# Performance work log

Hardware: AMD Instinct MI355X
Metric: run time of the kernel (lower is better)

## Reference

```python
import jax, jax.numpy as jnp
import numpy as np

B, S, D = 8, 2048, 1024
H = 2 * D  # FFN hidden
EPS = 1e-5

def _layernorm(x, gamma, beta):
    mu = jnp.mean(x, axis=-1, keepdims=True)
    var = jnp.mean(jnp.square(x - mu), axis=-1, keepdims=True)
    return (x - mu) * jax.lax.rsqrt(var + EPS) * gamma + beta

def setup_inputs() -> dict:
    key = jax.random.key(0)
    ks = jax.random.split(key, 9)
    s = 1.0 / np.sqrt(D)
    x = jax.random.normal(ks[0], (B, S, D), dtype=jnp.float32)
    Wq = jax.random.uniform(ks[1], (D, D), jnp.float32, -s, s)
    Wk = jax.random.uniform(ks[2], (D, D), jnp.float32, -s, s)
    Wv = jax.random.uniform(ks[3], (D, D), jnp.float32, -s, s)
    W1 = jax.random.uniform(ks[4], (H, D), jnp.float32, -s, s)
    b1 = jax.random.uniform(ks[5], (H,), jnp.float32, -s, s)
    s2 = 1.0 / np.sqrt(H)
    W2 = jax.random.uniform(ks[6], (D, H), jnp.float32, -s2, s2)
    b2 = jax.random.uniform(ks[7], (D,), jnp.float32, -s2, s2)
    g1 = jnp.ones((D,), jnp.float32); be1 = jnp.zeros((D,), jnp.float32)
    g2 = jnp.ones((D,), jnp.float32); be2 = jnp.zeros((D,), jnp.float32)
    return {"x": x, "Wq": Wq, "Wk": Wk, "Wv": Wv, "W1": W1, "b1": b1,
            "W2": W2, "b2": b2, "g1": g1, "be1": be1, "g2": g2, "be2": be2}

def reference(x, Wq, Wk, Wv, W1, b1, W2, b2, g1, be1, g2, be2):
    # q/k/v projections (torch Linear: x @ W.T)
    q = jnp.einsum('bsd,ed->bse', x, Wq)
    k = jnp.einsum('bsd,ed->bse', x, Wk)
    v = jnp.einsum('bsd,ed->bse', x, Wv)
    scores = jnp.einsum('bqd,bkd->bqk', q, k) / jnp.sqrt(jnp.float32(D))
    attn = jax.nn.softmax(scores, axis=-1)
    attn_out = jnp.einsum('bqk,bkd->bqd', attn, v)
    h = _layernorm(x + attn_out, g1, be1)
    ff = jnp.einsum('bsh,dh->bsd', jax.nn.relu(jnp.einsum('bsd,hd->bsh', h, W1) + b1), W2) + b2
    return _layernorm(h + ff, g2, be2)
```

## Files before the change

kernel.cpp:

```cpp
#include <hip/hip_runtime.h>
#include <hip/hip_bf16.h>


typedef __attribute__((ext_vector_type(4))) float  f32x4;
typedef __attribute__((ext_vector_type(8))) short  short8;
typedef __attribute__((ext_vector_type(4))) short  short4v;
typedef __attribute__((ext_vector_type(8))) __bf16 bf16x8;
typedef unsigned short ushort_t;

static __device__ __forceinline__ unsigned short f2bf(float f) {
  unsigned u = __builtin_bit_cast(unsigned, f);
  u += 0x7fffu + ((u >> 16) & 1u);
  return (unsigned short)(u >> 16);
}
static __device__ __forceinline__ float bf2f(unsigned short u) {
  return __builtin_bit_cast(float, (unsigned)u << 16);
}

#define GLDS16(g, l)                                                        \
  __builtin_amdgcn_global_load_lds(                                         \
      (const __attribute__((address_space(1))) void*)(g),                   \
      (__attribute__((address_space(3))) void*)(l), 16, 0, 0)

__global__ __launch_bounds__(256) void cvt_f32_bf16(
    const float* __restrict__ in, ushort_t* __restrict__ out, long n) {
  long i = ((long)blockIdx.x * 256 + threadIdx.x) * 8;
  if (i >= n) return;
  f32x4 a = *(const f32x4*)(in + i);
  f32x4 b = *(const f32x4*)(in + i + 4);
  short8 t;
  t[0] = (short)f2bf(a.x); t[1] = (short)f2bf(a.y);
  t[2] = (short)f2bf(a.z); t[3] = (short)f2bf(a.w);
  t[4] = (short)f2bf(b.x); t[5] = (short)f2bf(b.y);
  t[6] = (short)f2bf(b.z); t[7] = (short)f2bf(b.w);
  *(short8*)(out + i) = t;
}

enum { EP_QKV = 0, EP_BF16 = 1, EP_PV = 2, EP_FF1 = 3, EP_FF2 = 4 };

constexpr long BSDc = 8L * 2048 * 1024;

template <int EPI>
__global__ __launch_bounds__(512, 2) void gemm_bt(
    const ushort_t* __restrict__ A, const ushort_t* __restrict__ B,
    void* __restrict__ C, int N, int K, long sA, long sB, long sC, long sRes,
    const float* __restrict__ bias, const float* __restrict__ res,
    float scale) {
  __shared__ __align__(16) ushort_t As[4][8192];
  __shared__ __align__(16) ushort_t Bs[4][8192];
  const int tid  = threadIdx.x;
  const int lane = tid & 63;
  const int w    = tid >> 6;
  const int wm   = w >> 2;
  const int wn   = w & 3;
  const int l15  = lane & 15;
  const int hi   = lane >> 4;
  const long bz  = blockIdx.z;
  const long m0  = (long)blockIdx.x * 256;
  const long n0  = (long)blockIdx.y * 256;
  const ushort_t* Ab = A + bz * sA;
  const ushort_t* Bb = B + bz * sB;

  long aoff[2], boff[2];
#pragma unroll
  for (int q = 0; q < 2; ++q) {
    int P  = q * 512 + tid;
    int lr = P >> 3;
    int sl = (P & 7) ^ (lr & 7);
    int r  = 2 * lr + (sl >> 2);
    int kc = sl & 3;
    aoff[q] = (m0 + r) * (long)K + kc * 8;
    boff[q] = (n0 + r) * (long)K + kc * 8;
  }

#define STAGEA(u)                                                           \
  {                                                                         \
    const long kk0 = (long)(u) * 32;                                        \
    const int dbf  = (u) & 3;                                               \
    GLDS16(Ab + aoff[0] + kk0, &As[dbf][w * 512]);                          \
    GLDS16(Ab + aoff[1] + kk0, &As[dbf][4096 + w * 512]);                   \
  }
#define STAGEB(u)                                                           \
  {                                                                         \
    const long kk0 = (long)(u) * 32;                                        \
    const int dbf  = (u) & 3;                                               \
    GLDS16(Bb + boff[0] + kk0, &Bs[dbf][w * 512]);                          \
    GLDS16(Bb + boff[1] + kk0, &Bs[dbf][4096 + w * 512]);                   \
  }

  const int slotR = (((l15 & 1) << 2) | hi) ^ (l15 >> 1);
  const int abase = wm * 8192 + (l15 >> 1) * 128 + slotR * 16;
  const int bbase = wn * 4096 + (l15 >> 1) * 128 + slotR * 16;

  f32x4 acc[8][4] = {};
  const int NT = K >> 5;

  STAGEA(0) STAGEB(0) STAGEA(1) STAGEB(1) STAGEA(2) STAGEB(2)
  asm volatile("s_waitcnt vmcnt(8)" ::: "memory");
  __builtin_amdgcn_sched_barrier(0);
  __builtin_amdgcn_s_barrier();

  for (int u = 0; u < NT; ++u) {
    const int bf = u & 3;
    const char* Ad = (const char*)&As[bf][0];
    const char* Bd = (const char*)&Bs[bf][0];
    short8 af[8], bq[4];
#pragma unroll
    for (int i = 0; i < 4; ++i)
      af[i] = *(const short8*)(Ad + abase + i * 1024);
#pragma unroll
    for (int j = 0; j < 4; ++j)
      bq[j] = *(const short8*)(Bd + bbase + j * 1024);
    if (u + 3 < NT) STAGEA(u + 3)
    asm volatile("s_waitcnt lgkmcnt(0)" ::: "memory");
    __builtin_amdgcn_sched_barrier(0);
    __builtin_amdgcn_s_setprio(1);
#pragma unroll
    for (int i = 0; i < 4; ++i)
#pragma unroll
      for (int j = 0; j < 4; ++j)
        acc[i][j] = __builtin_amdgcn_mfma_f32_16x16x32_bf16(
            __builtin_bit_cast(bf16x8, af[i]), __builtin_bit_cast(bf16x8, bq[j]),
            acc[i][j], 0, 0, 0);
    __builtin_amdgcn_s_setprio(0);
    __builtin_amdgcn_sched_barrier(0);
    __builtin_amdgcn_s_barrier();
#pragma unroll
    for (int i = 4; i < 8; ++i)
      af[i] = *(const short8*)(Ad + abase + i * 1024);
    if (u + 3 < NT) STAGEB(u + 3)
    asm volatile("s_waitcnt lgkmcnt(0)" ::: "memory");
    __builtin_amdgcn_sched_barrier(0);
    __builtin_amdgcn_s_setprio(1);
#pragma unroll
    for (int i = 4; i < 8; ++i)
#pragma unroll
      for (int j = 0; j < 4; ++j)
        acc[i][j] = __builtin_amdgcn_mfma_f32_16x16x32_bf16(
            __builtin_bit_cast(bf16x8, af[i]), __builtin_bit_cast(bf16x8, bq[j]),
            acc[i][j], 0, 0, 0);
    __builtin_amdgcn_s_setprio(0);
    __builtin_amdgcn_sched_barrier(0);
    if (u + 1 < NT) {
      if (u + 3 < NT) {
        asm volatile("s_waitcnt vmcnt(8)" ::: "memory");
      } else if (u + 3 == NT) {
        asm volatile("s_waitcnt vmcnt(4)" ::: "memory");
      } else {
        asm volatile("s_waitcnt vmcnt(0)" ::: "memory");
      }
      __builtin_amdgcn_sched_barrier(0);
      __builtin_amdgcn_s_barrier();
    }
  }
#undef STAGEA
#undef STAGEB

  const int rb0 = hi << 2;
  const int cl  = l15;
#pragma unroll
  for (int i = 0; i < 8; ++i) {
#pragma unroll
    for (int j = 0; j < 4; ++j) {
      long gmb = m0 + wm * 128 + i * 16 + rb0;
      long gc  = n0 + wn * 64 + j * 16 + cl;
      if constexpr (EPI == EP_QKV) {
        long which = gc >> 10;
        long col   = gc & 1023;
        if (which == 2) {
          long bb = gmb >> 11, s = gmb & 2047;
          short4v pk;
#pragma unroll
          for (int r = 0; r < 4; ++r) pk[r] = (short)f2bf(acc[i][j][r]);
          *(short4v*)((ushort_t*)C + 2 * BSDc + ((bb << 10) + col) * 2048 + s) =
              pk;
        } else {
#pragma unroll
          for (int r = 0; r < 4; ++r)
            ((ushort_t*)C)[which * BSDc + (gmb + r) * 1024 + col] =
                f2bf(acc[i][j][r]);
        }
      } else {
#pragma unroll
        for (int r = 0; r < 4; ++r) {
          long gm = gmb + r;
          float v = acc[i][j][r] * scale;
          if constexpr (EPI == EP_BF16) {
            ((ushort_t*)C)[bz * sC + gm * N + gc] = f2bf(v);
          } else if constexpr (EPI == EP_PV) {
            v += res[bz * sRes + gm * N + gc];
            ((float*)C)[bz * sC + gm * N + gc] = v;
          } else if constexpr (EPI == EP_FF1) {
            v += bias[gc];
            v = v > 0.f ? v : 0.f;
            ((ushort_t*)C)[gm * N + gc] = f2bf(v);
          } else {
            v += bias[gc] + res[gm * N + gc];
            ((float*)C)[gm * N + gc] = v;
          }
        }
      }
    }
  }
}

__global__ __launch_bounds__(256) void softmax_inplace(
    ushort_t* __restrict__ P) {
  __shared__ float rmax[4], rsum[4];
  const int tid   = threadIdx.x;
  const long base = (long)blockIdx.x * 2048;
  short8 sv = *(const short8*)(P + base + tid * 8);
  float v[8];
#pragma unroll
  for (int j = 0; j < 8; ++j) v[j] = bf2f((unsigned short)sv[j]);
  float mx = v[0];
#pragma unroll
  for (int j = 1; j < 8; ++j) mx = fmaxf(mx, v[j]);
#pragma unroll
  for (int off = 32; off; off >>= 1) mx = fmaxf(mx, __shfl_down(mx, off, 64));
  if ((tid & 63) == 0) rmax[tid >> 6] = mx;
  __syncthreads();
  mx = fmaxf(fmaxf(rmax[0], rmax[1]), fmaxf(rmax[2], rmax[3]));
  float s = 0.f;
#pragma unroll
  for (int j = 0; j < 8; ++j) {
    v[j] = __expf(v[j] - mx);
    s += v[j];
  }
#pragma unroll
  for (int off = 32; off; off >>= 1) s += __shfl_down(s, off, 64);
  if ((tid & 63) == 0) rsum[tid >> 6] = s;
  __syncthreads();
  s = (rsum[0] + rsum[1]) + (rsum[2] + rsum[3]);
  float inv = 1.f / s;
  short8 o;
#pragma unroll
  for (int j = 0; j < 8; ++j) o[j] = (short)f2bf(v[j] * inv);
  *(short8*)(P + base + tid * 8) = o;
}

template <int MODE>
__global__ __launch_bounds__(256) void ln_row(const float* __restrict__ X,
                                              const float* __restrict__ g,
                                              const float* __restrict__ be,
                                              float* __restrict__ Yf,
                                              ushort_t* __restrict__ Yb) {
  __shared__ float rs[4], rq[4];
  const int tid   = threadIdx.x;
  const long base = (long)blockIdx.x << 10;
  f32x4 v = *(const f32x4*)(X + base + tid * 4);
  float s = v.x + v.y + v.z + v.w;
  float q = v.x * v.x + v.y * v.y + v.z * v.z + v.w * v.w;
#pragma unroll
  for (int off = 32; off; off >>= 1) {
    s += __shfl_down(s, off, 64);
    q += __shfl_down(q, off, 64);
  }
  if ((tid & 63) == 0) {
    rs[tid >> 6] = s;
    rq[tid >> 6] = q;
  }
  __syncthreads();
  s = (rs[0] + rs[1]) + (rs[2] + rs[3]);
  q = (rq[0] + rq[1]) + (rq[2] + rq[3]);
  float mu   = s * (1.f / 1024.f);
  float var  = q * (1.f / 1024.f) - mu * mu;
  float rstd = rsqrtf(var + 1e-5f);
  int c    = tid * 4;
  f32x4 gg = *(const f32x4*)(g + c);
  f32x4 bb = *(const f32x4*)(be + c);
  f32x4 y;
  y.x = (v.x - mu) * rstd * gg.x + bb.x;
  y.y = (v.y - mu) * rstd * gg.y + bb.y;
  y.z = (v.z - mu) * rstd * gg.z + bb.z;
  y.w = (v.w - mu) * rstd * gg.w + bb.w;
  *(f32x4*)(Yf + base + c) = y;
  if constexpr (MODE == 0) {
    short4v ob;
    ob[0] = (short)f2bf(y.x);
    ob[1] = (short)f2bf(y.y);
    ob[2] = (short)f2bf(y.z);
    ob[3] = (short)f2bf(y.w);
    *(short4v*)(Yb + base + c) = ob;
  }
}

extern "C" void kernel_launch(void* const* d_in, const int* in_sizes, int n_in,
                              void* d_out, int out_size, void* d_ws,
                              size_t ws_size, hipStream_t stream) {
  const float* x   = (const float*)d_in[0];
  const float* Wq  = (const float*)d_in[1];
  const float* Wk  = (const float*)d_in[2];
  const float* Wv  = (const float*)d_in[3];
  const float* W1  = (const float*)d_in[4];
  const float* b1  = (const float*)d_in[5];
  const float* W2  = (const float*)d_in[6];
  const float* b2  = (const float*)d_in[7];
  const float* g1  = (const float*)d_in[8];
  const float* be1 = (const float*)d_in[9];
  const float* g2  = (const float*)d_in[10];
  const float* be2 = (const float*)d_in[11];
  float* out = (float*)d_out;

  constexpr long BSD = 8L * 2048 * 1024;
  constexpr long BSS = 8L * 2048 * 2048;
  constexpr long DD  = 1024L * 1024;
  constexpr long HD  = 2048L * 1024;

  ushort_t* qb  = (ushort_t*)d_ws;
  ushort_t* kb  = qb + BSD;
  ushort_t* vTb = kb + BSD;
  ushort_t* sP  = vTb + BSD;
  float*    r1  = (float*)(sP + BSS);

  ushort_t* xb    = sP;
  ushort_t* Wqkvb = (ushort_t*)r1;
  ushort_t* W1b   = kb;
  ushort_t* W2b   = kb + HD;
  ushort_t* hb    = qb;
  float*    h     = out;

  dim3 blk(256), gblk(512);
  const long SD = 2048L * 1024, SS = 2048L * 2048, DS = 1024L * 2048;

  cvt_f32_bf16<<<dim3(8192), blk, 0, stream>>>(x, xb, BSD);
  cvt_f32_bf16<<<dim3(512), blk, 0, stream>>>(Wq, Wqkvb, DD);
  cvt_f32_bf16<<<dim3(512), blk, 0, stream>>>(Wk, Wqkvb + DD, DD);
  cvt_f32_bf16<<<dim3(512), blk, 0, stream>>>(Wv, Wqkvb + 2 * DD, DD);
  gemm_bt<EP_QKV><<<dim3(64, 12, 1), gblk, 0, stream>>>(
      xb, Wqkvb, qb, 3072, 1024, 0, 0, 0, 0, nullptr, nullptr, 1.f);
  gemm_bt<EP_BF16><<<dim3(8, 8, 8), gblk, 0, stream>>>(
      qb, kb, sP, 2048, 1024, SD, SD, SS, 0, nullptr, nullptr, 0.03125f);
  cvt_f32_bf16<<<dim3(1024), blk, 0, stream>>>(W1, W1b, HD);
  cvt_f32_bf16<<<dim3(1024), blk, 0, stream>>>(W2, W2b, HD);
  softmax_inplace<<<dim3(16384), blk, 0, stream>>>(sP);
  gemm_bt<EP_PV><<<dim3(8, 4, 8), gblk, 0, stream>>>(
      sP, vTb, r1, 1024, 2048, SS, DS, SD, SD, nullptr, x, 1.f);
  ln_row<0><<<dim3(16384), blk, 0, stream>>>(r1, g1, be1, h, hb);
  gemm_bt<EP_FF1><<<dim3(64, 8, 1), gblk, 0, stream>>>(
      hb, W1b, sP, 2048, 1024, 0, 0, 0, 0, b1, nullptr, 1.f);
  gemm_bt<EP_FF2><<<dim3(64, 4, 1), gblk, 0, stream>>>(
      sP, W2b, r1, 1024, 2048, 0, 0, 0, 0, b2, h, 1.f);
  ln_row<1><<<dim3(16384), blk, 0, stream>>>(r1, g2, be2, out, nullptr);
}
```

Baseline: 548.0 us.

## Software-pipeline LDS fragment loads across K tiles in GEMM main loop

Restructures the GEMM main loop so the A/B fragments for the next K tile are read from LDS while the second half of the current tile's MFMAs run, using register double buffering (AF0/BQ0, AF1/BQ1) and a loop unrolled by two. The second-half A fragments are issued before the first MFMA block with partial lgkmcnt waits. The goal is to hide LDS read latency behind matrix-core work. The cost is higher register pressure and a more intricate barrier and waitcnt ordering. The unroll by two assumes NT is even.

```diff
diff --git a/kernel.cpp b/kernel.cpp
--- a/kernel.cpp
+++ b/kernel.cpp
@@ -99,60 +99,89 @@
   asm volatile("s_waitcnt vmcnt(8)" ::: "memory");
   __builtin_amdgcn_sched_barrier(0);
   __builtin_amdgcn_s_barrier();
-
-  for (int u = 0; u < NT; ++u) {
-    const int bf = u & 3;
-    const char* Ad = (const char*)&As[bf][0];
-    const char* Bd = (const char*)&Bs[bf][0];
-    short8 af[8], bq[4];
+  __builtin_amdgcn_sched_barrier(0);
+
+  short8 AF0[4], BQ0[4], AF1[4], BQ1[4];
+  {
+    const char* Ad = (const char*)&As[0][0];
+    const char* Bd = (const char*)&Bs[0][0];
 #pragma unroll
     for (int i = 0; i < 4; ++i)
-      af[i] = *(const short8*)(Ad + abase + i * 1024);
+      AF0[i] = *(const short8*)(Ad + abase + i * 1024);
 #pragma unroll
     for (int j = 0; j < 4; ++j)
-      bq[j] = *(const short8*)(Bd + bbase + j * 1024);
-    if (u + 3 < NT) STAGEA(u + 3)
-    asm volatile("s_waitcnt lgkmcnt(0)" ::: "memory");
-    __builtin_amdgcn_sched_barrier(0);
-    __builtin_amdgcn_s_setprio(1);
-#pragma unroll
-    for (int i = 0; i < 4; ++i)
-#pragma unroll
-      for (int j = 0; j < 4; ++j)
-        acc[i][j] = __builtin_amdgcn_mfma_f32_16x16x32_bf16(
-            __builtin_bit_cast(bf16x8, af[i]), __builtin_bit_cast(bf16x8, bq[j]),
-            acc[i][j], 0, 0, 0);
-    __builtin_amdgcn_s_setprio(0);
-    __builtin_amdgcn_sched_barrier(0);
-    __builtin_amdgcn_s_barrier();
-#pragma unroll
-    for (int i = 4; i < 8; ++i)
-      af[i] = *(const short8*)(Ad + abase + i * 1024);
-    if (u + 3 < NT) STAGEB(u + 3)
-    asm volatile("s_waitcnt lgkmcnt(0)" ::: "memory");
-    __builtin_amdgcn_sched_barrier(0);
-    __builtin_amdgcn_s_setprio(1);
-#pragma unroll
-    for (int i = 4; i < 8; ++i)
-#pragma unroll
-      for (int j = 0; j < 4; ++j)
-        acc[i][j] = __builtin_amdgcn_mfma_f32_16x16x32_bf16(
-            __builtin_bit_cast(bf16x8, af[i]), __builtin_bit_cast(bf16x8, bq[j]),
-            acc[i][j], 0, 0, 0);
-    __builtin_amdgcn_s_setprio(0);
-    __builtin_amdgcn_sched_barrier(0);
-    if (u + 1 < NT) {
-      if (u + 3 < NT) {
-        asm volatile("s_waitcnt vmcnt(8)" ::: "memory");
-      } else if (u + 3 == NT) {
-        asm volatile("s_waitcnt vmcnt(4)" ::: "memory");
-      } else {
-        asm volatile("s_waitcnt vmcnt(0)" ::: "memory");
-      }
-      __builtin_amdgcn_sched_barrier(0);
-      __builtin_amdgcn_s_barrier();
-    }
-  }
+      BQ0[j] = *(const short8*)(Bd + bbase + j * 1024);
+  }
+
+#define TILE_BODY(u, AF, BQ, NAF, NBQ)                                      \
+  {                                                                         \
+    const char* Ad = (const char*)&As[(u) & 3][0];                          \
+    if ((u) + 3 < NT) STAGEA((u) + 3)                                       \
+    short8 fb0 = *(const short8*)(Ad + abase + 4096);                       \
+    short8 fb1 = *(const short8*)(Ad + abase + 5120);                       \
+    short8 fb2 = *(const short8*)(Ad + abase + 6144);                       \
+    short8 fb3 = *(const short8*)(Ad + abase + 7168);                       \
+    asm volatile("s_waitcnt lgkmcnt(4)" ::: "memory");                      \
+    __builtin_amdgcn_sched_barrier(0);                                      \
+    __builtin_amdgcn_s_setprio(1);                                          \
+    _Pragma("unroll") for (int i = 0; i < 4; ++i)                           \
+        _Pragma("unroll") for (int j = 0; j < 4; ++j)                       \
+            acc[i][j] = __builtin_amdgcn_mfma_f32_16x16x32_bf16(            \
+                __builtin_bit_cast(bf16x8, AF[i]),                          \
+                __builtin_bit_cast(bf16x8, BQ[j]), acc[i][j], 0, 0, 0);     \
+    __builtin_amdgcn_s_setprio(0);                                          \
+    __builtin_amdgcn_sched_barrier(0);                                      \
+    if ((u) + 3 < NT) STAGEB((u) + 3)                                       \
+    if ((u) + 1 < NT) {                                                     \
+      if ((u) + 3 < NT) {                                                   \
+        asm volatile("s_waitcnt vmcnt(8)" ::: "memory");                    \
+      } else if ((u) + 3 == NT) {                                           \
+        asm volatile("s_waitcnt vmcnt(4)" ::: "memory");                    \
+      } else {                                                              \
+        asm volatile("s_waitcnt vmcnt(0)" ::: "memory");                    \
+      }                                                                     \
+      __builtin_amdgcn_sched_barrier(0);                                    \
+      __builtin_amdgcn_s_barrier();       \
+      __builtin_amdgcn_sched_barrier(0);                                    \
+      const char* And = (const char*)&As[((u) + 1) & 3][0];                 \
+      const char* Bnd = (const char*)&Bs[((u) + 1) & 3][0];                 \
+      _Pragma("unroll") for (int i = 0; i < 4; ++i)                         \
+          NAF[i] = *(const short8*)(And + abase + i * 1024);                \
+      _Pragma("unroll") for (int j = 0; j < 4; ++j)                         \
+          NBQ[j] = *(const short8*)(Bnd + bbase + j * 1024);                \
+      asm volatile("s_waitcnt lgkmcnt(8)" ::: "memory");                    \
+    } else {                                                                \
+      asm volatile("s_waitcnt lgkmcnt(0)" ::: "memory");                    \
+    }                                                                       \
+    __builtin_amdgcn_sched_barrier(0);                                      \
+    __builtin_amdgcn_s_setprio(1);                                          \
+    _Pragma("unroll") for (int j = 0; j < 4; ++j) {                         \
+      acc[4][j] = __builtin_amdgcn_mfma_f32_16x16x32_bf16(                  \
+          __builtin_bit_cast(bf16x8, fb0), __builtin_bit_cast(bf16x8, BQ[j]),\
+          acc[4][j], 0, 0, 0);                                              \
+      acc[5][j] = __builtin_amdgcn_mfma_f32_16x16x32_bf16(                  \
+          __builtin_bit_cast(bf16x8, fb1), __builtin_bit_cast(bf16x8, BQ[j]),\
+          acc[5][j], 0, 0, 0);                                              \
+      acc[6][j] = __builtin_amdgcn_mfma_f32_16x16x32_bf16(                  \
+          __builtin_bit_cast(bf16x8, fb2), __builtin_bit_cast(bf16x8, BQ[j]),\
+          acc[6][j], 0, 0, 0);                                              \
+      acc[7][j] = __builtin_amdgcn_mfma_f32_16x16x32_bf16(                  \
+          __builtin_bit_cast(bf16x8, fb3), __builtin_bit_cast(bf16x8, BQ[j]),\
+          acc[7][j], 0, 0, 0);                                              \
+    }                                                                       \
+    __builtin_amdgcn_s_setprio(0);                                          \
+    __builtin_amdgcn_sched_barrier(0);                                      \
+    if ((u) + 1 < NT) {                                                     \
+      __builtin_amdgcn_s_barrier();  \
+      __builtin_amdgcn_sched_barrier(0);                                    \
+    }                                                                       \
+  }
+
+  for (int u = 0; u < NT; u += 2) {
+    TILE_BODY(u, AF0, BQ0, AF1, BQ1)
+    TILE_BODY(u + 1, AF1, BQ1, AF0, BQ0)
+  }
+#undef TILE_BODY
 #undef STAGEA
 #undef STAGEB
 
```

After: 589.9 us. 7.7% more time.
